# Kernel optimization log

Measured on AMD Instinct MI355X. Metric: run time of the kernel, lower is better.

Reference implementation:

```python
import jax, jax.numpy as jnp
import numpy as np

N = 50000        # nodes
E = 400000       # edges
IN_DIM = 128
HID = 64         # out_channels per head (concat=False -> mean over heads)
H = 4            # heads
C = HID          # per-head channels
HC = H * C
L = 6            # layers
EDIM = HID // 4  # edge embedding dim
NEG_SLOPE = 0.2


def setup_inputs() -> dict:
    key = jax.random.key(0)
    ks = jax.random.split(key, 16)
    s = 0.05
    return {
        "x": jax.random.normal(ks[0], (N, IN_DIM), dtype=jnp.float32),
        "edge_index": jax.random.randint(ks[1], (2, E), 0, N),
        "edge_attr": jax.random.randint(ks[2], (E,), 0, 3),
        "in_W": jax.random.normal(ks[3], (HID, IN_DIM), dtype=jnp.float32) * s,
        "in_b": jnp.zeros((HID,), jnp.float32),
        "edge_table": jax.random.normal(ks[4], (3, EDIM), dtype=jnp.float32) * s,
        "Wl": jax.random.normal(ks[5], (L, HC, HID), dtype=jnp.float32) * s,
        "bl": jnp.zeros((L, HC), jnp.float32),
        "Wr": jax.random.normal(ks[6], (L, HC, HID), dtype=jnp.float32) * s,
        "br": jnp.zeros((L, HC), jnp.float32),
        "We": jax.random.normal(ks[7], (L, HC, EDIM), dtype=jnp.float32) * s,
        "att": jax.random.normal(ks[8], (L, H, C), dtype=jnp.float32) * s,
        "out_bias": jnp.zeros((L, HID), jnp.float32),
        "ln_g": jnp.ones((L, HID), jnp.float32),
        "ln_b": jnp.zeros((L, HID), jnp.float32),
    }


def _layernorm(h, g, b):
    mu = h.mean(-1, keepdims=True)
    var = ((h - mu) ** 2).mean(-1, keepdims=True)
    return (h - mu) / jnp.sqrt(var + 1e-5) * g + b


def _gatv2_layer(h, src, dst, eemb, Wl, bl, Wr, br, We, att, bias):
    # GATv2Conv (PyG semantics, concat=False -> mean over heads), eval mode
    xl = (h @ Wl.T + bl).reshape(N, H, C)   # lin_l(x) -> source messages
    xr = (h @ Wr.T + br).reshape(N, H, C)   # lin_r(x) -> target term
    ep = (eemb @ We.T).reshape(E, H, C)     # lin_edge(edge_attr)
    m = xl[src] + xr[dst] + ep              # [E,H,C]
    s = jax.nn.leaky_relu(m, NEG_SLOPE)
    logit = jnp.einsum('ehc,hc->eh', s, att)  # [E,H]
    # segment softmax over incoming edges of each dst node
    mx = jax.ops.segment_max(logit, dst, num_segments=N)
    mx = jnp.where(jnp.isfinite(mx), mx, 0.0)
    ex = jnp.exp(logit - mx[dst])
    den = jax.ops.segment_sum(ex, dst, num_segments=N)
    alpha = ex / jnp.maximum(den[dst], 1e-16)           # [E,H]
    agg = jax.ops.segment_sum(xl[src] * alpha[:, :, None], dst, num_segments=N)  # [N,H,C]
    return agg.mean(axis=1) + bias          # concat=False -> head mean, then bias


def reference(x, edge_index, edge_attr, in_W, in_b, edge_table, Wl, bl, Wr, br,
              We, att, out_bias, ln_g, ln_b):
    h = x @ in_W.T + in_b                   # input projection [N,HID]
    eemb = edge_table[edge_attr]            # [E,EDIM]
    src, dst = edge_index[0], edge_index[1]
    use_res = [False] * (L // 2) + [True] * (L // 2)
    for i in range(L):
        h_in = h
        h = _gatv2_layer(h, src, dst, eemb, Wl[i], bl[i], Wr[i], br[i],
                         We[i], att[i], out_bias[i])
        h = _layernorm(h, ln_g[i], ln_b[i])
        if use_res[i]:
            h = h + h_in
        if i < L - 1:
            h = jax.nn.relu(h)  # dropout is identity in eval mode
    return h
```

## Files before the change

### kernel.cpp

```cpp
#include <hip/hip_runtime.h>
#include <hip/hip_bf16.h>
#include <hip/hip_fp16.h>
#include <math.h>

#define NN 50000
#define NE 400000
#define INDIM 128
#define HID 64
#define HC 256
#define NL 6
#define ED 16
#define SCAN_B 256
#define SCAN_NB ((NN + SCAN_B - 1)/SCAN_B)
#define NBIN 64
#define BINPAD 16

typedef __attribute__((ext_vector_type(8))) short short8;
typedef __attribute__((ext_vector_type(4))) float f32x4;
typedef _Float16 h2 __attribute__((ext_vector_type(2)));

static __device__ __forceinline__ float4 ld4(const float* p){ return *(const float4*)p; }
static __device__ __forceinline__ unsigned short f2b(float x){
  __hip_bfloat16 h = __float2bfloat16(x);
  return *(unsigned short*)&h;
}
static __device__ __forceinline__ unsigned short f2h(float x){
  __half h = __float2half(x);
  return *(unsigned short*)&h;
}
static __device__ __forceinline__ float b2f(unsigned short u){
  return __builtin_bit_cast(float, (unsigned)u << 16);
}

#define DPP_ADD(X, CTRL) \
  ((X) + __builtin_bit_cast(float, __builtin_amdgcn_update_dpp(0, __builtin_bit_cast(int, (X)), (CTRL), 0xF, 0xF, true)))

__global__ void prep_kernel(const float* __restrict__ inW, const float* __restrict__ Wl,
                            const float* __restrict__ Wr, const float* __restrict__ bl,
                            const float* __restrict__ br, const float* __restrict__ etab,
                            const float* __restrict__ We,
                            unsigned short* __restrict__ inW_bf,
                            unsigned short* __restrict__ Wlr,
                            float* __restrict__ blr, float* __restrict__ ep){
  int i = blockIdx.x*blockDim.x + threadIdx.x;
  if (i < HID*INDIM) inW_bf[i] = f2b(inW[i]);
  if (i < NL*512){
    int l = i / 512, c = i % 512;
    blr[i] = (c < HC) ? bl[l*HC + c] : br[l*HC + (c-HC)];
  }
  if (i < NL*3*HC){
    int l  = i / (3*HC);
    int a  = (i / HC) % 3;
    int hc = i % HC;
    const float* wrow = We + ((size_t)l*HC + hc)*ED;
    const float* erow = etab + a*ED;
    float s = 0.f;
    #pragma unroll
    for (int k=0;k<ED;k++) s += erow[k]*wrow[k];
    ep[i] = s;
  }
  int tot = NL*512*HID;
  for (int j = i; j < tot; j += gridDim.x*blockDim.x){
    int l = j / (512*HID);
    int c = (j / HID) % 512;
    int k = j % HID;
    float v = (c < HC) ? Wl[((size_t)l*HC + c)*HID + k]
                       : Wr[((size_t)l*HC + (c-HC))*HID + k];
    Wlr[j] = f2b(v);
  }
}

__global__ void deg_kernel(const int* __restrict__ dst, int* __restrict__ deg){
  int e = blockIdx.x*blockDim.x + threadIdx.x;
  if (e < NE) atomicAdd(&deg[dst[e]], 1);
}

__global__ void scanA_kernel(const int* __restrict__ deg, int* __restrict__ bsum){
  int t = threadIdx.x;
  int i = blockIdx.x*SCAN_B + t;
  int v = (i < NN) ? deg[i] : 0;
  #pragma unroll
  for (int o=1;o<64;o<<=1) v += __shfl_xor(v,o);
  __shared__ int ws[4];
  if ((t&63)==0) ws[t>>6] = v;
  __syncthreads();
  if (t==0) bsum[blockIdx.x] = ws[0]+ws[1]+ws[2]+ws[3];
}

__global__ void scanB_kernel(int* __restrict__ bsum){
  __shared__ int sh[256];
  int t = threadIdx.x;
  int v = (t < SCAN_NB) ? bsum[t] : 0;
  sh[t] = v;
  __syncthreads();
  for (int o=1;o<256;o<<=1){
    int u = (t>=o)?sh[t-o]:0;
    __syncthreads();
    sh[t]+=u;
    __syncthreads();
  }
  int excl = (t==0)?0:sh[t-1];
  if (t < SCAN_NB) bsum[t] = excl;
}

__global__ void scanC_kernel(const int* __restrict__ deg, const int* __restrict__ bsum,
                             int* __restrict__ rowp){
  int t = threadIdx.x, b = blockIdx.x;
  int i = b*SCAN_B + t;
  int v = (i<NN)?deg[i]:0;
  __shared__ int sh[256];
  sh[t]=v;
  __syncthreads();
  for (int o=1;o<256;o<<=1){
    int u=(t>=o)?sh[t-o]:0;
    __syncthreads();
    sh[t]+=u;
    __syncthreads();
  }
  if (i < NN) rowp[i] = bsum[b] + sh[t] - v;
  if (i == 0) rowp[NN] = NE;
}

__global__ void scatter_kernel(const int* __restrict__ src, const int* __restrict__ dst,
                               const int* __restrict__ attr, const int* __restrict__ rowp,
                               int* __restrict__ deg, int* __restrict__ csrp){
  int e = blockIdx.x*blockDim.x + threadIdx.x;
  if (e >= NE) return;
  int d = dst[e];
  int pos = rowp[d] + atomicSub(&deg[d], 1) - 1;
  csrp[pos] = src[e] | (attr[e] << 16);
}

__global__ void histE_kernel(const int* __restrict__ rowp, int* __restrict__ gbin,
                             int* __restrict__ bbase){
  __shared__ int lh[NBIN];
  int t = threadIdx.x, b = blockIdx.x;
  if (t < NBIN) lh[t] = 0;
  __syncthreads();
  int i = b*SCAN_B + t;
  if (i < NN){
    int dg = rowp[i+1] - rowp[i];
    if (dg > 63) dg = 63;
    atomicAdd(&lh[63 - dg], 1);
  }
  __syncthreads();
  if (t < NBIN){
    int c = lh[t];
    bbase[b*NBIN + t] = c ? atomicAdd(&gbin[t*BINPAD], c) : 0;
  }
}
__global__ void scanE_kernel(int* __restrict__ gbin){
  int t = threadIdx.x;
  int v = gbin[t*BINPAD];
  int s = v;
  #pragma unroll
  for (int o=1;o<64;o<<=1){
    int u = __shfl_up(s, o);
    if (t >= o) s += u;
  }
  gbin[t*BINPAD] = s - v;
}
__global__ void scatterE_kernel(const int* __restrict__ rowp, const int* __restrict__ gbin,
                                const int* __restrict__ bbase, int* __restrict__ order){
  __shared__ int lc[NBIN];
  int t = threadIdx.x, b = blockIdx.x;
  if (t < NBIN) lc[t] = 0;
  __syncthreads();
  int i = b*SCAN_B + t;
  if (i < NN){
    int dg = rowp[i+1] - rowp[i];
    if (dg > 63) dg = 63;
    int bin = 63 - dg;
    int r = atomicAdd(&lc[bin], 1);
    order[gbin[bin*BINPAD] + bbase[b*NBIN + bin] + r] = i;
  }
}

__global__ __launch_bounds__(256) void gemm_in_kernel(
    const float* __restrict__ X, const unsigned short* __restrict__ Wbf,
    const float* __restrict__ bias, unsigned short* __restrict__ hbf)
{
  int wid = threadIdx.x >> 6, lane = threadIdx.x & 63;
  int row0 = blockIdx.x*128 + wid*32;
  int lr = lane & 15, lk = lane >> 4;
  short8 a[2][4];
  #pragma unroll
  for (int rt=0; rt<2; rt++){
    int r = row0 + rt*16 + lr; if (r >= NN) r = NN-1;
    const float* rp = X + (size_t)r*INDIM;
    #pragma unroll
    for (int ks=0; ks<4; ks++){
      const float* p = rp + ks*32 + lk*8;
      float4 u = ld4(p), v = ld4(p+4);
      short8 t;
      t[0]=(short)f2b(u.x); t[1]=(short)f2b(u.y); t[2]=(short)f2b(u.z); t[3]=(short)f2b(u.w);
      t[4]=(short)f2b(v.x); t[5]=(short)f2b(v.y); t[6]=(short)f2b(v.z); t[7]=(short)f2b(v.w);
      a[rt][ks] = t;
    }
  }
  f32x4 acc[2][4] = {};
  #pragma unroll
  for (int ct=0; ct<4; ct++){
    int c = ct*16 + lr;
    #pragma unroll
    for (int ks=0; ks<4; ks++){
      short8 b = *(const short8*)&Wbf[(size_t)c*INDIM + ks*32 + lk*8];
      #pragma unroll
      for (int rt=0; rt<2; rt++)
        acc[rt][ct] = __builtin_amdgcn_mfma_f32_16x16x32_bf16(a[rt][ks], b, acc[rt][ct], 0,0,0);
    }
  }
  #pragma unroll
  for (int rt=0; rt<2; rt++)
    #pragma unroll
    for (int ct=0; ct<4; ct++){
      int c = ct*16 + lr;
      float bv = bias[c];
      #pragma unroll
      for (int q=0;q<4;q++){
        int r = row0 + rt*16 + lk*4 + q;
        if (r < NN) hbf[(size_t)r*HID + c] = f2b(acc[rt][ct][q] + bv);
      }
    }
}

__global__ __launch_bounds__(256) void gemm_lr_kernel(
    const unsigned short* __restrict__ Abf, const unsigned short* __restrict__ Wbf,
    const float* __restrict__ bias, unsigned short* __restrict__ out)
{
  int wid = threadIdx.x >> 6, lane = threadIdx.x & 63;
  int row0 = blockIdx.x*128 + wid*32;
  int col0 = blockIdx.y*64;
  int lr = lane & 15, lk = lane >> 4;
  short8 a[2][2];
  #pragma unroll
  for (int rt=0; rt<2; rt++){
    int r = row0 + rt*16 + lr; if (r >= NN) r = NN-1;
    #pragma unroll
    for (int ks=0; ks<2; ks++)
      a[rt][ks] = *(const short8*)&Abf[(size_t)r*HID + ks*32 + lk*8];
  }
  f32x4 acc[2][4] = {};
  #pragma unroll
  for (int ct=0; ct<4; ct++){
    int c = col0 + ct*16 + lr;
    #pragma unroll
    for (int ks=0; ks<2; ks++){
      short8 b = *(const short8*)&Wbf[(size_t)c*HID + ks*32 + lk*8];
      #pragma unroll
      for (int rt=0; rt<2; rt++)
        acc[rt][ct] = __builtin_amdgcn_mfma_f32_16x16x32_bf16(a[rt][ks], b, acc[rt][ct], 0,0,0);
    }
  }
  #pragma unroll
  for (int rt=0; rt<2; rt++)
    #pragma unroll
    for (int ct=0; ct<4; ct++){
      int c = col0 + ct*16 + lr;
      float bv = bias[c];
      #pragma unroll
      for (int q=0;q<4;q++){
        int r = row0 + rt*16 + lk*4 + q;
        if (r < NN) out[(size_t)r*512 + c] = f2h(acc[rt][ct][q] + bv);
      }
    }
}

#define EDGE_BODY(UX, UY, A)                                                   \
  {                                                                            \
    h2 x2a = __builtin_bit_cast(h2, (UX));                                     \
    h2 x2b = __builtin_bit_cast(h2, (UY));                                     \
    h2 m2a = x2a + ((A)==0 ? xre0a : ((A)==1 ? xre1a : xre2a));                \
    h2 m2b = x2b + ((A)==0 ? xre0b : ((A)==1 ? xre1b : xre2b));                \
    h2 n2a = __builtin_bit_cast(h2, __builtin_bit_cast(unsigned, m2a) & 0x7FFF7FFFu); \
    h2 n2b = __builtin_bit_cast(h2, __builtin_bit_cast(unsigned, m2b) & 0x7FFF7FFFu); \
    float part = __builtin_amdgcn_fdot2(m2a, av6a, 0.f, false);                \
    part = __builtin_amdgcn_fdot2(m2b, av6b, part, false);                     \
    part = __builtin_amdgcn_fdot2(n2a, av4a, part, false);                     \
    part = __builtin_amdgcn_fdot2(n2b, av4b, part, false);                     \
    part = DPP_ADD(part, 0xB1);                                                \
    part = DPP_ADD(part, 0x4E);                                                \
    part = DPP_ADD(part, 0x124);                                               \
    part = DPP_ADD(part, 0x128);                                               \
    float p = exp2f(part);                                                     \
    den += p;                                                                  \
    ax = fmaf(p, (float)x2a.x, ax);                                            \
    ay = fmaf(p, (float)x2a.y, ay);                                            \
    az = fmaf(p, (float)x2b.x, az);                                            \
    aw = fmaf(p, (float)x2b.y, aw);                                            \
  }

__global__ __launch_bounds__(256) void agg_kernel(
    const unsigned short* __restrict__ xlr,
    const int* __restrict__ rowp, const int* __restrict__ csrp,
    const int* __restrict__ order,
    const float* __restrict__ ep_l, const float* __restrict__ att_l,
    const float* __restrict__ bias_l, const float* __restrict__ g_l, const float* __restrict__ b_l,
    unsigned short* __restrict__ hbf, float* __restrict__ out_last,
    int use_res, int do_relu, int last)
{
  int idx = (blockIdx.x << 2) | (threadIdx.x >> 6);
  int lane = threadIdx.x & 63;
  if (idx >= NN) return;
  int d = order[idx];
  int cb = lane << 2;

  uint2 xru = *(const uint2*)(xlr + ((size_t)d << 9) + 256 + cb);
  h2 xr2a = __builtin_bit_cast(h2, xru.x);
  h2 xr2b = __builtin_bit_cast(h2, xru.y);
  float xrf0 = (float)xr2a.x, xrf1 = (float)xr2a.y;
  float xrf2 = (float)xr2b.x, xrf3 = (float)xr2b.y;

  float4 ev0 = ld4(ep_l + cb);
  float4 ev1 = ld4(ep_l + HC + cb);
  float4 ev2 = ld4(ep_l + 2*HC + cb);
  h2 xre0a = {(_Float16)(xrf0+ev0.x), (_Float16)(xrf1+ev0.y)};
  h2 xre0b = {(_Float16)(xrf2+ev0.z), (_Float16)(xrf3+ev0.w)};
  h2 xre1a = {(_Float16)(xrf0+ev1.x), (_Float16)(xrf1+ev1.y)};
  h2 xre1b = {(_Float16)(xrf2+ev1.z), (_Float16)(xrf3+ev1.w)};
  h2 xre2a = {(_Float16)(xrf0+ev2.x), (_Float16)(xrf1+ev2.y)};
  h2 xre2b = {(_Float16)(xrf2+ev2.z), (_Float16)(xrf3+ev2.w)};

  float4 av = ld4(att_l + cb);
  const float K6 = 0.6f*1.44269504f, K4 = 0.4f*1.44269504f;
  h2 av6a = {(_Float16)(av.x*K6), (_Float16)(av.y*K6)};
  h2 av6b = {(_Float16)(av.z*K6), (_Float16)(av.w*K6)};
  h2 av4a = {(_Float16)(av.x*K4), (_Float16)(av.y*K4)};
  h2 av4b = {(_Float16)(av.z*K4), (_Float16)(av.w*K4)};

  float den = 0.f;
  float ax=0.f, ay=0.f, az=0.f, aw=0.f;

  int beg = rowp[d], stop = rowp[d+1];
  int i = beg;
  for (; i + 4 <= stop; i += 4){
    int p0 = csrp[i], p1 = csrp[i+1], p2 = csrp[i+2], p3 = csrp[i+3];
    uint2 u0 = *(const uint2*)(xlr + ((size_t)(p0 & 0xFFFF) << 9) + cb);
    uint2 u1 = *(const uint2*)(xlr + ((size_t)(p1 & 0xFFFF) << 9) + cb);
    uint2 u2 = *(const uint2*)(xlr + ((size_t)(p2 & 0xFFFF) << 9) + cb);
    uint2 u3 = *(const uint2*)(xlr + ((size_t)(p3 & 0xFFFF) << 9) + cb);
    int a0 = p0 >> 16, a1 = p1 >> 16, a2 = p2 >> 16, a3 = p3 >> 16;
    EDGE_BODY(u0.x, u0.y, a0);
    EDGE_BODY(u1.x, u1.y, a1);
    EDGE_BODY(u2.x, u2.y, a2);
    EDGE_BODY(u3.x, u3.y, a3);
  }
  if (i + 2 <= stop){
    int p0 = csrp[i], p1 = csrp[i+1];
    uint2 u0 = *(const uint2*)(xlr + ((size_t)(p0 & 0xFFFF) << 9) + cb);
    uint2 u1 = *(const uint2*)(xlr + ((size_t)(p1 & 0xFFFF) << 9) + cb);
    int a0 = p0 >> 16, a1 = p1 >> 16;
    EDGE_BODY(u0.x, u0.y, a0);
    EDGE_BODY(u1.x, u1.y, a1);
    i += 2;
  }
  if (i < stop){
    int p0 = csrp[i];
    uint2 u0 = *(const uint2*)(xlr + ((size_t)(p0 & 0xFFFF) << 9) + cb);
    int a0 = p0 >> 16;
    EDGE_BODY(u0.x, u0.y, a0);
  }

  float inv = (den > 0.f) ? 1.f/den : 0.f;
  ax *= inv; ay *= inv; az *= inv; aw *= inv;

  ax += __shfl_xor(ax,16); ay += __shfl_xor(ay,16); az += __shfl_xor(az,16); aw += __shfl_xor(aw,16);
  ax += __shfl_xor(ax,32); ay += __shfl_xor(ay,32); az += __shfl_xor(az,32); aw += __shfl_xor(aw,32);

  int cc = (lane & 15) << 2;
  float4 bv = ld4(bias_l + cc);
  float h0 = ax*0.25f + bv.x;
  float h1 = ay*0.25f + bv.y;
  float h2v = az*0.25f + bv.z;
  float h3 = aw*0.25f + bv.w;

  float s1 = h0+h1+h2v+h3;
  float s2 = h0*h0 + h1*h1 + h2v*h2v + h3*h3;
  s1 += __shfl_xor(s1,1); s2 += __shfl_xor(s2,1);
  s1 += __shfl_xor(s1,2); s2 += __shfl_xor(s2,2);
  s1 += __shfl_xor(s1,4); s2 += __shfl_xor(s2,4);
  s1 += __shfl_xor(s1,8); s2 += __shfl_xor(s2,8);
  float mu  = s1 * (1.f/64.f);
  float var = fmaxf(s2*(1.f/64.f) - mu*mu, 0.f);
  float rstd = rsqrtf(var + 1e-5f);
  float4 gv  = ld4(g_l + cc);
  float4 bbv = ld4(b_l + cc);
  float r0 = (h0-mu)*rstd*gv.x + bbv.x;
  float r1 = (h1-mu)*rstd*gv.y + bbv.y;
  float r2 = (h2v-mu)*rstd*gv.z + bbv.z;
  float r3 = (h3-mu)*rstd*gv.w + bbv.w;
  if (use_res){
    ushort4 hv = *(const ushort4*)(hbf + (size_t)d*HID + cc);
    r0 += b2f(hv.x); r1 += b2f(hv.y); r2 += b2f(hv.z); r3 += b2f(hv.w);
  }
  if (do_relu){
    r0 = fmaxf(r0, 0.f); r1 = fmaxf(r1, 0.f);
    r2 = fmaxf(r2, 0.f); r3 = fmaxf(r3, 0.f);
  }
  if (lane < 16){
    if (last){
      float4 o = {r0, r1, r2, r3};
      *(float4*)(out_last + (size_t)d*HID + cc) = o;
    } else {
      ushort4 obv = {f2b(r0), f2b(r1), f2b(r2), f2b(r3)};
      *(ushort4*)(hbf + (size_t)d*HID + cc) = obv;
    }
  }
}

extern "C" void kernel_launch(void* const* d_in, const int* in_sizes, int n_in,
                              void* d_out, int out_size, void* d_ws, size_t ws_size,
                              hipStream_t stream){
  const float* x    = (const float*)d_in[0];
  const int*   ei   = (const int*)d_in[1];
  const int*   ea   = (const int*)d_in[2];
  const float* inW  = (const float*)d_in[3];
  const float* inb  = (const float*)d_in[4];
  const float* etab = (const float*)d_in[5];
  const float* Wl   = (const float*)d_in[6];
  const float* bl   = (const float*)d_in[7];
  const float* Wr   = (const float*)d_in[8];
  const float* br   = (const float*)d_in[9];
  const float* We   = (const float*)d_in[10];
  const float* att  = (const float*)d_in[11];
  const float* ob   = (const float*)d_in[12];
  const float* lg   = (const float*)d_in[13];
  const float* lb   = (const float*)d_in[14];

  char* w = (char*)d_ws;
  size_t off = 0;
  auto alloc = [&](size_t bytes)->char*{
    char* p = w + off;
    off = (off + bytes + 255) & ~(size_t)255;
    return p;
  };
  unsigned short* hbf = (unsigned short*)alloc((size_t)NN*HID*2);
  unsigned short* xlr = (unsigned short*)alloc((size_t)NN*512*2);
  unsigned short* inW_bf = (unsigned short*)alloc((size_t)HID*INDIM*2);
  unsigned short* Wlr    = (unsigned short*)alloc((size_t)NL*512*HID*2);
  float* blr   = (float*)alloc((size_t)NL*512*4);
  float* ep    = (float*)alloc((size_t)NL*3*HC*4);
  int*   deg   = (int*)alloc((size_t)NN*4);
  int*   bsum  = (int*)alloc((size_t)SCAN_NB*4);
  int*   rowp  = (int*)alloc((size_t)(NN+1)*4);
  int*   csrp  = (int*)alloc((size_t)NE*4);
  int*   gbin  = (int*)alloc((size_t)NBIN*BINPAD*4);
  int*   bbase = (int*)alloc((size_t)SCAN_NB*NBIN*4);
  int*   order = (int*)alloc((size_t)NN*4);

  hipMemsetAsync(deg, 0, (size_t)NN*4, stream);
  hipMemsetAsync(gbin, 0, (size_t)NBIN*BINPAD*4, stream);

  const int* srcp = ei;
  const int* dstp = ei + NE;
  deg_kernel<<<dim3((NE+255)/256), dim3(256), 0, stream>>>(dstp, deg);
  scanA_kernel<<<dim3(SCAN_NB), dim3(256), 0, stream>>>(deg, bsum);
  scanB_kernel<<<dim3(1), dim3(256), 0, stream>>>(bsum);
  scanC_kernel<<<dim3(SCAN_NB), dim3(256), 0, stream>>>(deg, bsum, rowp);
  scatter_kernel<<<dim3((NE+255)/256), dim3(256), 0, stream>>>(srcp, dstp, ea, rowp, deg, csrp);
  histE_kernel<<<dim3(SCAN_NB), dim3(256), 0, stream>>>(rowp, gbin, bbase);
  scanE_kernel<<<dim3(1), dim3(64), 0, stream>>>(gbin);
  scatterE_kernel<<<dim3(SCAN_NB), dim3(256), 0, stream>>>(rowp, gbin, bbase, order);
  prep_kernel<<<dim3(64), dim3(256), 0, stream>>>(inW, Wl, Wr, bl, br, etab, We, inW_bf, Wlr, blr, ep);

  const int MB = (NN + 127)/128;
  gemm_in_kernel<<<dim3(MB), dim3(256), 0, stream>>>(x, inW_bf, inb, hbf);

  for (int l=0; l<NL; l++){
    gemm_lr_kernel<<<dim3(MB,8), dim3(256), 0, stream>>>(
        hbf, Wlr + (size_t)l*512*HID, blr + (size_t)l*512, xlr);
    agg_kernel<<<dim3((NN+3)/4), dim3(256), 0, stream>>>(
        xlr, rowp, csrp, order,
        ep + (size_t)l*3*HC, att + (size_t)l*HC,
        ob + (size_t)l*HID, lg + (size_t)l*HID, lb + (size_t)l*HID,
        hbf, (float*)d_out,
        (l >= NL/2) ? 1 : 0, (l < NL-1) ? 1 : 0, (l == NL-1) ? 1 : 0);
  }
}
```

Measured before the change: 542.0 us.

## Fuse degree-bin ordering into CSR scans and vectorize GEMM epilogue stores

The degree-histogram, bin-scan and order-scatter kernels are merged into the existing scanA/scanB/scanC kernels, and the gbin memset is folded into deg_kernel. This removes three kernel launches and one memset from the preprocessing chain. Separately, both MFMA GEMMs swap operand order so each lane holds four consecutive output columns, which allows vector stores with float4 bias loads instead of scattered 2-byte stores. One risk: scanC's lc[] reset is not followed by a barrier before its atomics, although the scan's later __syncthreads likely covers it.

Measured after the change: 523.3 us. -3.4%, faster.

```diff
diff --git a/kernel.cpp b/kernel.cpp
--- a/kernel.cpp
+++ b/kernel.cpp
@@ -70,24 +70,39 @@
   }
 }
 
-__global__ void deg_kernel(const int* __restrict__ dst, int* __restrict__ deg){
+__global__ void deg_kernel(const int* __restrict__ dst, int* __restrict__ deg,
+                           int* __restrict__ gbin){
   int e = blockIdx.x*blockDim.x + threadIdx.x;
+  if (e < NBIN*BINPAD) gbin[e] = 0;
   if (e < NE) atomicAdd(&deg[dst[e]], 1);
 }
 
-__global__ void scanA_kernel(const int* __restrict__ deg, int* __restrict__ bsum){
-  int t = threadIdx.x;
-  int i = blockIdx.x*SCAN_B + t;
+__global__ void scanA_kernel(const int* __restrict__ deg, int* __restrict__ bsum,
+                             int* __restrict__ gbin, int* __restrict__ bbase){
+  __shared__ int lh[NBIN];
+  __shared__ int ws[4];
+  int t = threadIdx.x, b = blockIdx.x;
+  if (t < NBIN) lh[t] = 0;
+  __syncthreads();
+  int i = b*SCAN_B + t;
   int v = (i < NN) ? deg[i] : 0;
-  #pragma unroll
-  for (int o=1;o<64;o<<=1) v += __shfl_xor(v,o);
-  __shared__ int ws[4];
-  if ((t&63)==0) ws[t>>6] = v;
+  if (i < NN){
+    int dg = v > 63 ? 63 : v;
+    atomicAdd(&lh[63 - dg], 1);
+  }
+  int s = v;
+  #pragma unroll
+  for (int o=1;o<64;o<<=1) s += __shfl_xor(s,o);
+  if ((t&63)==0) ws[t>>6] = s;
   __syncthreads();
-  if (t==0) bsum[blockIdx.x] = ws[0]+ws[1]+ws[2]+ws[3];
-}
-
-__global__ void scanB_kernel(int* __restrict__ bsum){
+  if (t==0) bsum[b] = ws[0]+ws[1]+ws[2]+ws[3];
+  if (t < NBIN){
+    int c = lh[t];
+    bbase[b*NBIN + t] = c ? atomicAdd(&gbin[t*BINPAD], c) : 0;
+  }
+}
+
+__global__ void scanB_kernel(int* __restrict__ bsum, int* __restrict__ gbin){
   __shared__ int sh[256];
   int t = threadIdx.x;
   int v = (t < SCAN_NB) ? bsum[t] : 0;
@@ -101,14 +116,27 @@
   }
   int excl = (t==0)?0:sh[t-1];
   if (t < SCAN_NB) bsum[t] = excl;
+  if (t < NBIN){
+    int v2 = gbin[t*BINPAD];
+    int s2 = v2;
+    #pragma unroll
+    for (int o=1;o<64;o<<=1){
+      int u = __shfl_up(s2, o);
+      if (t >= o) s2 += u;
+    }
+    gbin[t*BINPAD] = s2 - v2;
+  }
 }
 
 __global__ void scanC_kernel(const int* __restrict__ deg, const int* __restrict__ bsum,
-                             int* __restrict__ rowp){
+                             const int* __restrict__ gbin, const int* __restrict__ bbase,
+                             int* __restrict__ rowp, int* __restrict__ order){
+  __shared__ int sh[256];
+  __shared__ int lc[NBIN];
   int t = threadIdx.x, b = blockIdx.x;
+  if (t < NBIN) lc[t] = 0;
   int i = b*SCAN_B + t;
   int v = (i<NN)?deg[i]:0;
-  __shared__ int sh[256];
   sh[t]=v;
   __syncthreads();
   for (int o=1;o<256;o<<=1){
@@ -119,6 +147,12 @@
   }
   if (i < NN) rowp[i] = bsum[b] + sh[t] - v;
   if (i == 0) rowp[NN] = NE;
+  if (i < NN){
+    int dg = v > 63 ? 63 : v;
+    int bin = 63 - dg;
+    int r = atomicAdd(&lc[bin], 1);
+    order[gbin[bin*BINPAD] + bbase[b*NBIN + bin] + r] = i;
+  }
 }
 
 __global__ void scatter_kernel(const int* __restrict__ src, const int* __restrict__ dst,
@@ -131,51 +165,6 @@
   csrp[pos] = src[e] | (attr[e] << 16);
 }
 
-__global__ void histE_kernel(const int* __restrict__ rowp, int* __restrict__ gbin,
-                             int* __restrict__ bbase){
-  __shared__ int lh[NBIN];
-  int t = threadIdx.x, b = blockIdx.x;
-  if (t < NBIN) lh[t] = 0;
-  __syncthreads();
-  int i = b*SCAN_B + t;
-  if (i < NN){
-    int dg = rowp[i+1] - rowp[i];
-    if (dg > 63) dg = 63;
-    atomicAdd(&lh[63 - dg], 1);
-  }
-  __syncthreads();
-  if (t < NBIN){
-    int c = lh[t];
-    bbase[b*NBIN + t] = c ? atomicAdd(&gbin[t*BINPAD], c) : 0;
-  }
-}
-__global__ void scanE_kernel(int* __restrict__ gbin){
-  int t = threadIdx.x;
-  int v = gbin[t*BINPAD];
-  int s = v;
-  #pragma unroll
-  for (int o=1;o<64;o<<=1){
-    int u = __shfl_up(s, o);
-    if (t >= o) s += u;
-  }
-  gbin[t*BINPAD] = s - v;
-}
-__global__ void scatterE_kernel(const int* __restrict__ rowp, const int* __restrict__ gbin,
-                                const int* __restrict__ bbase, int* __restrict__ order){
-  __shared__ int lc[NBIN];
-  int t = threadIdx.x, b = blockIdx.x;
-  if (t < NBIN) lc[t] = 0;
-  __syncthreads();
-  int i = b*SCAN_B + t;
-  if (i < NN){
-    int dg = rowp[i+1] - rowp[i];
-    if (dg > 63) dg = 63;
-    int bin = 63 - dg;
-    int r = atomicAdd(&lc[bin], 1);
-    order[gbin[bin*BINPAD] + bbase[b*NBIN + bin] + r] = i;
-  }
-}
-
 __global__ __launch_bounds__(256) void gemm_in_kernel(
     const float* __restrict__ X, const unsigned short* __restrict__ Wbf,
     const float* __restrict__ bias, unsigned short* __restrict__ hbf)
@@ -207,21 +196,23 @@
       short8 b = *(const short8*)&Wbf[(size_t)c*INDIM + ks*32 + lk*8];
       #pragma unroll
       for (int rt=0; rt<2; rt++)
-        acc[rt][ct] = __builtin_amdgcn_mfma_f32_16x16x32_bf16(a[rt][ks], b, acc[rt][ct], 0,0,0);
-    }
-  }
-  #pragma unroll
-  for (int rt=0; rt<2; rt++)
-    #pragma unroll
-    for (int ct=0; ct<4; ct++){
-      int c = ct*16 + lr;
-      float bv = bias[c];
+        acc[rt][ct] = __builtin_amdgcn_mfma_f32_16x16x32_bf16(b, a[rt][ks], acc[rt][ct], 0,0,0);
+    }
+  }
+  #pragma unroll
+  for (int rt=0; rt<2; rt++){
+    int r = row0 + rt*16 + lr;
+    if (r < NN){
       #pragma unroll
-      for (int q=0;q<4;q++){
-        int r = row0 + rt*16 + lk*4 + q;
-        if (r < NN) hbf[(size_t)r*HID + c] = f2b(acc[rt][ct][q] + bv);
+      for (int ct=0; ct<4; ct++){
+        int cq = ct*16 + (lk<<2);
+        float4 bv = ld4(bias + cq);
+        ushort4 o = { f2b(acc[rt][ct][0]+bv.x), f2b(acc[rt][ct][1]+bv.y),
+                      f2b(acc[rt][ct][2]+bv.z), f2b(acc[rt][ct][3]+bv.w) };
+        *(ushort4*)&hbf[(size_t)r*HID + cq] = o;
       }
     }
+  }
 }
 
 __global__ __launch_bounds__(256) void gemm_lr_kernel(
@@ -249,21 +240,24 @@
       short8 b = *(const short8*)&Wbf[(size_t)c*HID + ks*32 + lk*8];
       #pragma unroll
       for (int rt=0; rt<2; rt++)
-        acc[rt][ct] = __builtin_amdgcn_mfma_f32_16x16x32_bf16(a[rt][ks], b, acc[rt][ct], 0,0,0);
-    }
-  }
-  #pragma unroll
-  for (int rt=0; rt<2; rt++)
-    #pragma unroll
-    for (int ct=0; ct<4; ct++){
-      int c = col0 + ct*16 + lr;
-      float bv = bias[c];
+        acc[rt][ct] = __builtin_amdgcn_mfma_f32_16x16x32_bf16(b, a[rt][ks], acc[rt][ct], 0,0,0);
+    }
+  }
+  #pragma unroll
+  for (int rt=0; rt<2; rt++){
+    int r = row0 + rt*16 + lr;
+    if (r < NN){
       #pragma unroll
-      for (int q=0;q<4;q++){
-        int r = row0 + rt*16 + lk*4 + q;
-        if (r < NN) out[(size_t)r*512 + c] = f2h(acc[rt][ct][q] + bv);
+      for (int ct=0; ct<4; ct++){
+        int cq = col0 + ct*16 + (lk<<2);
+        float4 bv = ld4(bias + cq);
+        unsigned lo = (unsigned)f2h(acc[rt][ct][0]+bv.x) | ((unsigned)f2h(acc[rt][ct][1]+bv.y)<<16);
+        unsigned hi = (unsigned)f2h(acc[rt][ct][2]+bv.z) | ((unsigned)f2h(acc[rt][ct][3]+bv.w)<<16);
+        uint2 o = {lo, hi};
+        *(uint2*)&out[(size_t)r*512 + cq] = o;
       }
     }
+  }
 }
 
 #define EDGE_BODY(UX, UY, A)                                                   \
@@ -449,18 +443,14 @@
   int*   order = (int*)alloc((size_t)NN*4);
 
   hipMemsetAsync(deg, 0, (size_t)NN*4, stream);
-  hipMemsetAsync(gbin, 0, (size_t)NBIN*BINPAD*4, stream);
 
   const int* srcp = ei;
   const int* dstp = ei + NE;
-  deg_kernel<<<dim3((NE+255)/256), dim3(256), 0, stream>>>(dstp, deg);
-  scanA_kernel<<<dim3(SCAN_NB), dim3(256), 0, stream>>>(deg, bsum);
-  scanB_kernel<<<dim3(1), dim3(256), 0, stream>>>(bsum);
-  scanC_kernel<<<dim3(SCAN_NB), dim3(256), 0, stream>>>(deg, bsum, rowp);
+  deg_kernel<<<dim3((NE+255)/256), dim3(256), 0, stream>>>(dstp, deg, gbin);
+  scanA_kernel<<<dim3(SCAN_NB), dim3(256), 0, stream>>>(deg, bsum, gbin, bbase);
+  scanB_kernel<<<dim3(1), dim3(256), 0, stream>>>(bsum, gbin);
+  scanC_kernel<<<dim3(SCAN_NB), dim3(256), 0, stream>>>(deg, bsum, gbin, bbase, rowp, order);
   scatter_kernel<<<dim3((NE+255)/256), dim3(256), 0, stream>>>(srcp, dstp, ea, rowp, deg, csrp);
-  histE_kernel<<<dim3(SCAN_NB), dim3(256), 0, stream>>>(rowp, gbin, bbase);
-  scanE_kernel<<<dim3(1), dim3(64), 0, stream>>>(gbin);
-  scatterE_kernel<<<dim3(SCAN_NB), dim3(256), 0, stream>>>(rowp, gbin, bbase, order);
   prep_kernel<<<dim3(64), dim3(256), 0, stream>>>(inW, Wl, Wr, bl, br, etab, We, inW_bf, Wlr, blr, ep);
 
   const int MB = (NN + 127)/128;
```
